# Performance work log

Measured on AMD Instinct MI355X. Metric: run time of the kernel, lower is better.

The kernel has to match this reference:

```python
import jax, jax.numpy as jnp
import numpy as np

TEMPERATURE = 0.07
EPS = 1e-12  # F.normalize eps


def _l2norm(x):
    n = jnp.linalg.norm(x, axis=-1, keepdims=True)
    return x / jnp.maximum(n, EPS)


def setup_inputs() -> dict:
    key = jax.random.key(0)
    k1, k2 = jax.random.split(key)
    B, T, H = 16, 512, 1024
    h_source = jax.random.normal(k1, (B, T, H), dtype=jnp.float32)
    h_target = jax.random.normal(k2, (B, T, H), dtype=jnp.float32)
    src_mask = jnp.ones((B, T), dtype=bool)
    tgt_mask = jnp.ones((B, T), dtype=bool)
    return {"h_source": h_source, "h_target": h_target,
            "src_mask": src_mask, "tgt_mask": tgt_mask}


def reference(h_source, h_target, src_mask, tgt_mask):
    # Masks are all-True and B*T == max_samples, so boolean selection == reshape
    # and the random subsampling branch is never taken (deterministic path).
    H = h_source.shape[-1]
    h_s = h_source.reshape(-1, H).astype(jnp.float32)          # (N, H)
    h_t = jax.lax.stop_gradient(h_target.reshape(-1, H)).astype(jnp.float32)  # detached

    h_s_norm = _l2norm(h_s)                                     # (N, H)
    h_t_norm = _l2norm(h_t)                                     # (M, H)
    sim = h_s_norm @ h_t_norm.T                                 # (N, M) cosine sim

    pos_idx = jnp.argmax(sim, axis=1)                           # == topk_idx[:, 0]
    logits = sim / TEMPERATURE
    # cross-entropy with pos_idx labels (stable log-softmax)
    logp = jax.nn.log_softmax(logits, axis=1)
    l_contrastive = -jnp.mean(jnp.take_along_axis(logp, pos_idx[:, None], axis=1)[:, 0])

    # contextual consistency: adjacent source tokens' NN embeddings should align
    nn_embeds = h_t_norm[pos_idx]                               # (N, H)
    nn_sim = jnp.sum(nn_embeds[:-1] * nn_embeds[1:], axis=-1)   # (N-1,)
    l_contextual = 1.0 - jnp.mean(nn_sim)

    return (l_contrastive, l_contextual)
```

## Files before the change

kernel.cpp:

```cpp
#include <hip/hip_runtime.h>
#include <hip/hip_bf16.h>
#include <stdint.h>


#define HDIM 1024
#define NROW 8192
#define TEMP_INV (1.0f / 0.07f)

typedef __attribute__((ext_vector_type(4))) float float4v;
typedef __attribute__((ext_vector_type(2))) float float2v;

#define SN_OFF   ((size_t)0)
#define TN_OFF   ((size_t)8388608)
#define TR_OFF   ((size_t)16777216)
#define SUM_OFF  ((size_t)25165824)
#define PMX_OFF  (SUM_OFF + 32768)
#define ACC_OFF  (PMX_OFF + 65536)
#define CNT_OFF  (ACC_OFF + 64)

static __device__ __forceinline__ void gload_lds16(const void* gptr, void* lptr) {
    __builtin_amdgcn_global_load_lds(
        (const __attribute__((address_space(1))) void*)gptr,
        (__attribute__((address_space(3))) void*)(uintptr_t)(uint32_t)(uintptr_t)lptr,
        16, 0, 0);
}

static __device__ __forceinline__ float fp8dot4(unsigned a, unsigned b) {
    float2v al = __builtin_amdgcn_cvt_pk_f32_fp8((int)a, false);
    float2v ah = __builtin_amdgcn_cvt_pk_f32_fp8((int)a, true);
    float2v bl = __builtin_amdgcn_cvt_pk_f32_fp8((int)b, false);
    float2v bh = __builtin_amdgcn_cvt_pk_f32_fp8((int)b, true);
    return al[0]*bl[0] + al[1]*bl[1] + ah[0]*bh[0] + ah[1]*bh[1];
}

__global__ __launch_bounds__(256)
void norm_kernel(const float* __restrict__ hs, const float* __restrict__ ht,
                 char* __restrict__ Sn, char* __restrict__ Tn, char* __restrict__ Tr,
                 float* __restrict__ sumexp, unsigned long long* __restrict__ pmax,
                 float* __restrict__ acc, unsigned* __restrict__ cnt) {
    const int b = blockIdx.x;
    const int t = threadIdx.x;
    const int wave = t >> 6, lane = t & 63;
    const bool isT = (b >= 512);
    const int g = isT ? (b - 512) : b;
    const float* in = (isT ? ht : hs) + (size_t)g * 16 * HDIM;
    char* outTiled = (isT ? Tn : Sn) + (size_t)g * 16384;

    __shared__ float sq[16][256];
    __shared__ float sscale[16];

    float4v v[16];
    #pragma unroll
    for (int i = 0; i < 16; ++i) {
        v[i] = ((const float4v*)in)[i * 256 + t];
        sq[i][t] = v[i][0]*v[i][0] + v[i][1]*v[i][1] + v[i][2]*v[i][2] + v[i][3]*v[i][3];
    }
    __syncthreads();
    #pragma unroll
    for (int j = 0; j < 4; ++j) {
        const int ri = wave * 4 + j;
        float s = sq[ri][lane] + sq[ri][lane + 64] + sq[ri][lane + 128] + sq[ri][lane + 192];
        #pragma unroll
        for (int off = 1; off < 64; off <<= 1) s += __shfl_xor(s, off);
        if (lane == 0) sscale[ri] = 1.0f / fmaxf(sqrtf(s), 1e-12f);
    }
    __syncthreads();

    char* tiled = (char*)sq;
    const int koff = (t >> 3) * 512 + ((t >> 1) & 3) * 128 + (t & 1) * 4;
    #pragma unroll
    for (int i = 0; i < 16; ++i) {
        const float sc = sscale[i];
        int d = __builtin_amdgcn_cvt_pk_fp8_f32(v[i][0]*sc, v[i][1]*sc, 0, false);
        d     = __builtin_amdgcn_cvt_pk_fp8_f32(v[i][2]*sc, v[i][3]*sc, d, true);
        *(int*)(tiled + koff + i * 8) = d;
        if (isT) ((int*)(Tr + (size_t)(g * 16 + i) * HDIM))[t] = d;
    }
    __syncthreads();
    #pragma unroll
    for (int j = 0; j < 4; ++j)
        ((uint4*)outTiled)[j * 256 + t] = ((const uint4*)tiled)[j * 256 + t];

    if (!isT && t < 16) { sumexp[b * 16 + t] = 0.f; pmax[b * 16 + t] = 0ull; }
    if (b == 0 && t == 16) { acc[0] = 0.f; acc[1] = 0.f; *cnt = 0u; }
}

__global__ __launch_bounds__(512, 4)
void flash_kernel(const char* __restrict__ Sn, const char* __restrict__ Tn,
                  float* __restrict__ sumexp, unsigned long long* __restrict__ pmax) {
    __shared__ __align__(16) char As[16384];
    __shared__ __align__(16) char Bs[8192];
    __shared__ float stSe[256];
    __shared__ unsigned long long stPk[256];
    const int t = threadIdx.x;
    const int wave = t >> 6, lane = t & 63;
    const int quad = lane >> 4, l16 = lane & 15;
    const int rbase  = (int)(blockIdx.x & 31) * 256;
    const int cbase0 = (int)(blockIdx.x >> 5) * 256;

    if (t < 256) { stSe[t] = 0.f; stPk[t] = 0ull; }

    const int wm = (wave & 3) * 64, wn = (wave >> 2) * 64;
    const char* gaBase0 = Sn + (size_t)(rbase / 16 + wave * 2 + 0) * 16384 + lane * 16;
    const char* gaBase1 = Sn + (size_t)(rbase / 16 + wave * 2 + 1) * 16384 + lane * 16;

    for (int s = 0; s < 2; ++s) {
        const int cbase = cbase0 + s * 128;
        const char* ga0 = gaBase0;
        const char* ga1 = gaBase1;
        const char* gb  = Tn + (size_t)(cbase / 16 + wave) * 16384 + lane * 16;

        float4v acc[4][4];
        #pragma unroll
        for (int i = 0; i < 4; ++i)
            #pragma unroll
            for (int j = 0; j < 4; ++j) acc[i][j] = (float4v){0.f, 0.f, 0.f, 0.f};

        for (int kb = 0; kb < 16; ++kb) {
            gload_lds16(ga0, As + (wave * 2 + 0) * 1024);
            gload_lds16(ga1, As + (wave * 2 + 1) * 1024);
            gload_lds16(gb,  Bs + wave * 1024);
            ga0 += 1024; ga1 += 1024; gb += 1024;
            __syncthreads();
            #pragma unroll
            for (int ks = 0; ks < 2; ++ks) {
                long af[4], bf[4];
                #pragma unroll
                for (int i = 0; i < 4; ++i)
                    af[i] = *(const long*)(As + ((wave & 3) * 4 + i) * 1024 + ks * 512 + lane * 8);
                #pragma unroll
                for (int j = 0; j < 4; ++j)
                    bf[j] = *(const long*)(Bs + ((wave >> 2) * 4 + j) * 1024 + ks * 512 + lane * 8);
                #pragma unroll
                for (int i = 0; i < 4; ++i)
                    #pragma unroll
                    for (int j = 0; j < 4; ++j)
                        acc[i][j] = __builtin_amdgcn_mfma_f32_16x16x32_fp8_fp8(af[i], bf[j], acc[i][j], 0, 0, 0);
            }
            __syncthreads();
        }

        float* pbSe = (float*)Bs;
        unsigned long long* pbPk = (unsigned long long*)(Bs + 1024);
        float se_v[4][4]; unsigned long long pk_v[4][4];
        #pragma unroll
        for (int i = 0; i < 4; ++i) {
            #pragma unroll
            for (int r = 0; r < 4; ++r) {
                float se = 0.f; float mx = -2.f; int mi = 0x7fffffff;
                #pragma unroll
                for (int j = 0; j < 4; ++j) {
                    float v = acc[i][j][r];
                    se += __expf(v * TEMP_INV);
                    int col = cbase + wn + j * 16 + l16;
                    if (v > mx || (v == mx && col < mi)) { mx = v; mi = col; }
                }
                #pragma unroll
                for (int off = 1; off < 16; off <<= 1) {
                    se += __shfl_xor(se, off);
                    float om = __shfl_xor(mx, off);
                    int oi = __shfl_xor(mi, off);
                    if (om > mx || (om == mx && oi < mi)) { mx = om; mi = oi; }
                }
                se_v[i][r] = se;
                pk_v[i][r] = ((unsigned long long)__float_as_uint(mx + 2.0f) << 32)
                             | (unsigned long long)(0xffffffffu - (unsigned)mi);
            }
        }
        if (wave < 4 && l16 == 0) {
            #pragma unroll
            for (int i = 0; i < 4; ++i)
                #pragma unroll
                for (int r = 0; r < 4; ++r) {
                    int rl = wm + i * 16 + quad * 4 + r;
                    pbSe[rl] = se_v[i][r]; pbPk[rl] = pk_v[i][r];
                }
        }
        __syncthreads();
        if (wave >= 4 && l16 == 0) {
            #pragma unroll
            for (int i = 0; i < 4; ++i)
                #pragma unroll
                for (int r = 0; r < 4; ++r) {
                    int rl = wm + i * 16 + quad * 4 + r;
                    float se = se_v[i][r] + pbSe[rl];
                    unsigned long long pk = pk_v[i][r];
                    unsigned long long po = pbPk[rl];
                    if (po > pk) pk = po;
                    stSe[rl] += se;
                    if (pk > stPk[rl]) stPk[rl] = pk;
                }
        }
        __syncthreads();
    }

    if (t < 256) {
        atomicAdd(&sumexp[rbase + t], stSe[t]);
        atomicMax(&pmax[rbase + t], stPk[t]);
    }
}

__global__ __launch_bounds__(256)
void tail_kernel(const float* __restrict__ sumexp,
                 const unsigned long long* __restrict__ pmax,
                 const char* __restrict__ Tr,
                 float* __restrict__ acc, unsigned* __restrict__ cnt,
                 float* __restrict__ out) {
    const int blk = blockIdx.x;
    const int t = threadIdx.x, wave = t >> 6, lane = t & 63;

    if (wave == 0) {
        int r = blk * 32 + (lane & 31);
        unsigned long long p = pmax[r];
        float mx = __uint_as_float((unsigned)(p >> 32)) - 2.0f;
        float loss = logf(sumexp[r]) - mx * TEMP_INV;
        #pragma unroll
        for (int off = 1; off < 32; off <<= 1) loss += __shfl_xor(loss, off);
        if (lane == 0) atomicAdd(acc + 0, loss);
    }

    float s = 0.f;
    #pragma unroll
    for (int it = 0; it < 8; ++it) {
        int g = blk * 32 + wave * 8 + it;
        if (g < NROW - 1) {
            unsigned long long pa = pmax[g], pb = pmax[g + 1];
            int ia = (int)(0xffffffffu - (unsigned)(pa & 0xffffffffu));
            int ib = (int)(0xffffffffu - (unsigned)(pb & 0xffffffffu));
            uint4 va = ((const uint4*)(Tr + (size_t)ia * HDIM))[lane];
            uint4 vb = ((const uint4*)(Tr + (size_t)ib * HDIM))[lane];
            s += fp8dot4(va.x, vb.x) + fp8dot4(va.y, vb.y)
               + fp8dot4(va.z, vb.z) + fp8dot4(va.w, vb.w);
        }
    }
    #pragma unroll
    for (int off = 1; off < 64; off <<= 1) s += __shfl_xor(s, off);
    __shared__ float red[4];
    if (lane == 0) red[wave] = s;
    __syncthreads();
    if (t == 0) atomicAdd(acc + 1, red[0] + red[1] + red[2] + red[3]);

    __threadfence();
    __shared__ unsigned done;
    if (t == 0) done = atomicAdd(cnt, 1u);
    __syncthreads();
    if (t == 0 && done == 255u) {
        float l0 = atomicAdd(acc + 0, 0.0f);
        float l1 = atomicAdd(acc + 1, 0.0f);
        out[0] = l0 / (float)NROW;
        out[1] = 1.0f - l1 / (float)(NROW - 1);
    }
}

extern "C" void kernel_launch(void* const* d_in, const int* in_sizes, int n_in,
                              void* d_out, int out_size, void* d_ws, size_t ws_size,
                              hipStream_t stream) {
    const float* hs = (const float*)d_in[0];
    const float* ht = (const float*)d_in[1];
    char* ws = (char*)d_ws;
    char* Sn = ws + SN_OFF;
    char* Tn = ws + TN_OFF;
    char* Tr = ws + TR_OFF;
    float* sumexp = (float*)(ws + SUM_OFF);
    unsigned long long* pmax = (unsigned long long*)(ws + PMX_OFF);
    float* acc = (float*)(ws + ACC_OFF);
    unsigned* cnt = (unsigned*)(ws + CNT_OFF);
    float* out = (float*)d_out;

    norm_kernel<<<1024, 256, 0, stream>>>(hs, ht, Sn, Tn, Tr, sumexp, pmax, acc, cnt);
    flash_kernel<<<1024, 512, 0, stream>>>(Sn, Tn, sumexp, pmax);
    tail_kernel<<<256, 256, 0, stream>>>(sumexp, pmax, Tr, acc, cnt, out);
}
```

Baseline: 260.5 us.

## Double-buffer LDS tiles in flash kernel to overlap global loads with MFMA

Splits the A and B shared-memory tiles into two buffers. The next k-block, and the first block of the second column pass, is prefetched into the alternate buffer while MFMAs run on the current one, and one barrier per iteration is dropped. The epilogue scratch arrays move to dedicated shared arrays so they no longer alias Bs. This doubles LDS use per block, which may lower occupancy under the 4-block launch bound. The global_load_lds writes may also need explicit vmcnt waits that a plain __syncthreads might not provide.

Result: slower. 267.9 us (+2.8%).

```diff
diff --git a/kernel.cpp b/kernel.cpp
--- a/kernel.cpp
+++ b/kernel.cpp
@@ -88,8 +88,10 @@
 __global__ __launch_bounds__(512, 4)
 void flash_kernel(const char* __restrict__ Sn, const char* __restrict__ Tn,
                   float* __restrict__ sumexp, unsigned long long* __restrict__ pmax) {
-    __shared__ __align__(16) char As[16384];
-    __shared__ __align__(16) char Bs[8192];
+    __shared__ __align__(16) char As[2][16384];
+    __shared__ __align__(16) char Bs[2][8192];
+    __shared__ float pbSe[256];
+    __shared__ unsigned long long pbPk[256];
     __shared__ float stSe[256];
     __shared__ unsigned long long stPk[256];
     const int t = threadIdx.x;
@@ -101,14 +103,18 @@
     if (t < 256) { stSe[t] = 0.f; stPk[t] = 0ull; }
 
     const int wm = (wave & 3) * 64, wn = (wave >> 2) * 64;
-    const char* gaBase0 = Sn + (size_t)(rbase / 16 + wave * 2 + 0) * 16384 + lane * 16;
-    const char* gaBase1 = Sn + (size_t)(rbase / 16 + wave * 2 + 1) * 16384 + lane * 16;
+    const char* ga0 = Sn + (size_t)(rbase / 16 + wave * 2 + 0) * 16384 + lane * 16;
+    const char* ga1 = Sn + (size_t)(rbase / 16 + wave * 2 + 1) * 16384 + lane * 16;
+    const char* gbs[2];
+    gbs[0] = Tn + (size_t)((cbase0 +   0) / 16 + wave) * 16384 + lane * 16;
+    gbs[1] = Tn + (size_t)((cbase0 + 128) / 16 + wave) * 16384 + lane * 16;
+
+    gload_lds16(ga0,    &As[0][(wave * 2 + 0) * 1024]);
+    gload_lds16(ga1,    &As[0][(wave * 2 + 1) * 1024]);
+    gload_lds16(gbs[0], &Bs[0][wave * 1024]);
 
     for (int s = 0; s < 2; ++s) {
         const int cbase = cbase0 + s * 128;
-        const char* ga0 = gaBase0;
-        const char* ga1 = gaBase1;
-        const char* gb  = Tn + (size_t)(cbase / 16 + wave) * 16384 + lane * 16;
 
         float4v acc[4][4];
         #pragma unroll
@@ -117,31 +123,34 @@
             for (int j = 0; j < 4; ++j) acc[i][j] = (float4v){0.f, 0.f, 0.f, 0.f};
 
         for (int kb = 0; kb < 16; ++kb) {
-            gload_lds16(ga0, As + (wave * 2 + 0) * 1024);
-            gload_lds16(ga1, As + (wave * 2 + 1) * 1024);
-            gload_lds16(gb,  Bs + wave * 1024);
-            ga0 += 1024; ga1 += 1024; gb += 1024;
+            const int p = kb & 1;
             __syncthreads();
+            if (kb < 15) {
+                gload_lds16(ga0 + (kb + 1) * 1024,    &As[1 - p][(wave * 2 + 0) * 1024]);
+                gload_lds16(ga1 + (kb + 1) * 1024,    &As[1 - p][(wave * 2 + 1) * 1024]);
+                gload_lds16(gbs[s] + (kb + 1) * 1024, &Bs[1 - p][wave * 1024]);
+            } else if (s == 0) {
+                gload_lds16(ga0,    &As[0][(wave * 2 + 0) * 1024]);
+                gload_lds16(ga1,    &As[0][(wave * 2 + 1) * 1024]);
+                gload_lds16(gbs[1], &Bs[0][wave * 1024]);
+            }
             #pragma unroll
             for (int ks = 0; ks < 2; ++ks) {
                 long af[4], bf[4];
                 #pragma unroll
                 for (int i = 0; i < 4; ++i)
-                    af[i] = *(const long*)(As + ((wave & 3) * 4 + i) * 1024 + ks * 512 + lane * 8);
+                    af[i] = *(const long*)(&As[p][((wave & 3) * 4 + i) * 1024 + ks * 512 + lane * 8]);
                 #pragma unroll
                 for (int j = 0; j < 4; ++j)
-                    bf[j] = *(const long*)(Bs + ((wave >> 2) * 4 + j) * 1024 + ks * 512 + lane * 8);
+                    bf[j] = *(const long*)(&Bs[p][((wave >> 2) * 4 + j) * 1024 + ks * 512 + lane * 8]);
                 #pragma unroll
                 for (int i = 0; i < 4; ++i)
                     #pragma unroll
                     for (int j = 0; j < 4; ++j)
                         acc[i][j] = __builtin_amdgcn_mfma_f32_16x16x32_fp8_fp8(af[i], bf[j], acc[i][j], 0, 0, 0);
             }
-            __syncthreads();
-        }
-
-        float* pbSe = (float*)Bs;
-        unsigned long long* pbPk = (unsigned long long*)(Bs + 1024);
+        }
+
         float se_v[4][4]; unsigned long long pk_v[4][4];
         #pragma unroll
         for (int i = 0; i < 4; ++i) {
```
